# Kernel optimization log

Measured on AMD Instinct MI355X. Metric: run time of the kernel, lower is better.

The kernel has to match this reference:

```python
import jax, jax.numpy as jnp
import numpy as np

N_HEADS = 4
T_OUT = 24  # total T; y has T - t_in steps


def setup_inputs() -> dict:
    key = jax.random.key(0)
    k1, k2, k3, k4 = jax.random.split(key, 4)
    B, t_in, N, C, K = 2, 12, 10000, 16, 17  # K = k + 1 (self)
    x = jax.random.normal(k1, (B, t_in, N, C), dtype=jnp.float32)
    nearest_nodes = jax.random.randint(k2, (N, K), 0, N, dtype=jnp.int32)
    nearest_dists = jax.random.uniform(k3, (N, K), dtype=jnp.float32)
    shrink_w = jax.random.normal(k4, (T_OUT - t_in, t_in * N_HEADS), dtype=jnp.float32) * 0.1
    shrink_b = jnp.zeros((T_OUT - t_in,), dtype=jnp.float32)
    return {"x": x, "nearest_nodes": nearest_nodes, "nearest_dists": nearest_dists,
            "shrink_w": shrink_w, "shrink_b": shrink_b}


def reference(x, nearest_nodes, nearest_dists, shrink_w, shrink_b):
    B, t_in, N, C = x.shape
    H = N_HEADS
    # sigma = nearest_dists.max() / sigma_ratio, with sigma_ratio = 1
    sigma = jnp.max(nearest_dists)
    lam = jnp.arange(1, H + 1, dtype=x.dtype) / H  # (H,)
    # distance weights per head: (N, K, H)
    w = jnp.exp(-(nearest_dists[..., None] ** 2) * lam / (sigma ** 2))
    w = jnp.where((nearest_nodes == -1)[..., None], 0.0, w)
    w = jnp.where(w < 1e-8, 0.0, w)
    # pad node at index N; -1 neighbors map to pad (weight already zero)
    pad_x = jnp.concatenate([x, jnp.zeros_like(x[:, :, :1])], axis=2)  # (B,T,N+1,C)
    idx = jnp.where(nearest_nodes == -1, N, nearest_nodes)  # (N, K)
    g = pad_x[:, :, idx]  # (B, t_in, N, K, C) neighbor gather
    # weighted reduce over neighbor axis -> (B, t_in, N, H, C)
    agg = jnp.einsum('btnkc,nkh->btnhc', g, w)
    # (B, N, C, t_in*H)
    a = jnp.transpose(agg, (0, 2, 4, 1, 3)).reshape(B, N, C, t_in * H)
    y = a @ shrink_w.T + shrink_b  # (B, N, C, T - t_in)
    y = jnp.transpose(y, (0, 3, 1, 2))  # (B, T - t_in, N, C)
    y = jax.nn.selu(y)  # CustomActivationFunction default mode='selu'
    return jnp.concatenate([x, y], axis=1)  # (B, T, N, C)
```

## Files before the change

kernel.cpp:

```cpp
#include <hip/hip_runtime.h>
#include <hip/hip_bf16.h>
#include <math.h>

#define NB      2
#define T_IN    12
#define T_OUT_  24
#define O_OUT   12
#define NN      10000
#define CC      16
#define KK      17
#define HH      4
#define JJ      48
#define PL      24
#define XCHN    40
#define CHN     250
#define XBLK    (PL * XCHN)
#define SBLK    167
#define GN      8
#define GBLK    (NN / GN)
#define PSTRU   34
#define ANSU    (PL * PSTRU)

__device__ __forceinline__ unsigned int f2bf(float f) {
    union { float f; unsigned int u; } v; v.f = f;
    unsigned int r = v.u + 0x7FFFu + ((v.u >> 16) & 1u);
    return r >> 16;
}
__device__ __forceinline__ float bf_lo(unsigned int u) {
    union { unsigned int u; float f; } v; v.u = u << 16; return v.f;
}
__device__ __forceinline__ float bf_hi(unsigned int u) {
    union { unsigned int u; float f; } v; v.u = u & 0xffff0000u; return v.f;
}

__global__ __launch_bounds__(256) void setup_kernel(
    const float* __restrict__ x,
    const float* __restrict__ dists, int ndists,
    float* __restrict__ out,
    unsigned short* __restrict__ xt,
    int* __restrict__ sigma_bits)
{
    const int tid = threadIdx.x;
    if (blockIdx.x < XBLK) {
        const int p  = blockIdx.x / XCHN;
        const int ch = blockIdx.x % XCHN;
        const int b = p / T_IN, t = p % T_IN;
        const int n0 = ch * CHN;
        const float* xp = x + (long)(p * NN + n0) * CC;
        float* op = out + (long)((b * T_OUT_ + t) * NN + n0) * CC;
        uint2* xtp = (uint2*)xt + (long)n0 * (PL * 4) + p * 4;
        for (int i = tid; i < CHN * 4; i += 256) {
            const int nl = i >> 2, q = i & 3;
            const float4 v = *(const float4*)(xp + i * 4);
            *(float4*)(op + i * 4) = v;
            uint2 pk;
            pk.x = f2bf(v.x) | (f2bf(v.y) << 16);
            pk.y = f2bf(v.z) | (f2bf(v.w) << 16);
            xtp[(long)nl * (PL * 4) + q] = pk;
        }
    } else {
        const int sb = blockIdx.x - XBLK;
        float m = 0.0f;
        const int nv4 = ndists >> 2;
        const float4* d4 = (const float4*)dists;
        for (int i = sb * 256 + tid; i < nv4; i += SBLK * 256) {
            float4 v = d4[i];
            m = fmaxf(fmaxf(m, fmaxf(v.x, v.y)), fmaxf(v.z, v.w));
        }
        for (int i = (nv4 << 2) + sb * 256 + tid; i < ndists; i += SBLK * 256)
            m = fmaxf(m, dists[i]);
        #pragma unroll
        for (int off = 32; off > 0; off >>= 1)
            m = fmaxf(m, __shfl_down(m, off, 64));
        __shared__ float sm[4];
        int lane = tid & 63, wid = tid >> 6;
        if (lane == 0) sm[wid] = m;
        __syncthreads();
        if (tid == 0) {
            float mm = fmaxf(fmaxf(sm[0], sm[1]), fmaxf(sm[2], sm[3]));
            atomicMax(sigma_bits, __float_as_int(mm));
        }
    }
}

__global__ __launch_bounds__(384) void fused_kernel(
    const unsigned short* __restrict__ xt,
    const int*   __restrict__ nodes,
    const float* __restrict__ dists,
    const int*   __restrict__ sigma_bits,
    const float* __restrict__ Wm,
    const float* __restrict__ bias,
    float* __restrict__ out)
{
    const int tid = threadIdx.x;
    const int n0  = blockIdx.x * GN;

    __shared__ int      lidx[GN * KK];
    __shared__ float    lw[GN * KK][HH];
    __shared__ float    W_s[O_OUT * JJ];
    __shared__ float    b_s[O_OUT];
    __shared__ unsigned a_s[GN * ANSU];

    for (int i = tid; i < O_OUT * JJ; i += 384) W_s[i] = Wm[i];
    if (tid < O_OUT) b_s[tid] = bias[tid];

    const float sigma  = __int_as_float(*sigma_bits);
    const float inv_s2 = 1.0f / (sigma * sigma);
    if (tid < GN * KK) {
        const int   nd = nodes[n0 * KK + tid];
        const float dd = dists[n0 * KK + tid];
        const float e1 = expf(-dd * dd * inv_s2 * 0.25f);
        float w0 = e1, w1 = e1 * e1, w2 = w1 * e1, w3 = w1 * w1;
        if (nd == -1) { w0 = w1 = w2 = w3 = 0.f; }
        if (w0 < 1e-8f) w0 = 0.f;
        if (w1 < 1e-8f) w1 = 0.f;
        if (w2 < 1e-8f) w2 = 0.f;
        if (w3 < 1e-8f) w3 = 0.f;
        lidx[tid]  = ((nd < 0) ? 0 : nd) * (PL * CC * 2);
        lw[tid][0] = w0; lw[tid][1] = w1; lw[tid][2] = w2; lw[tid][3] = w3;
    }
    __syncthreads();

    const int slot  = tid / 48;
    const int l     = tid % 48;
    const int rb    = slot * KK;
    const int plane = l >> 1;
    const int co    = (l & 1) * 8;
    const char* xtb = (const char*)xt;

    float acc[HH][8];
    #pragma unroll
    for (int h = 0; h < HH; ++h)
        #pragma unroll
        for (int j = 0; j < 8; ++j) acc[h][j] = 0.f;

    #pragma unroll
    for (int k = 0; k < KK; ++k) {
        const uint4  gv = *(const uint4*)(xtb + lidx[rb + k] + (l << 4));
        const float4 wv = *(const float4*)lw[rb + k];
        float g[8];
        g[0] = bf_lo(gv.x); g[1] = bf_hi(gv.x);
        g[2] = bf_lo(gv.y); g[3] = bf_hi(gv.y);
        g[4] = bf_lo(gv.z); g[5] = bf_hi(gv.z);
        g[6] = bf_lo(gv.w); g[7] = bf_hi(gv.w);
        #pragma unroll
        for (int j = 0; j < 8; ++j) {
            acc[0][j] += g[j] * wv.x;
            acc[1][j] += g[j] * wv.y;
            acc[2][j] += g[j] * wv.z;
            acc[3][j] += g[j] * wv.w;
        }
    }

    {
        unsigned* ap = a_s + slot * ANSU + plane * PSTRU + co * 2;
        #pragma unroll
        for (int j = 0; j < 8; ++j) {
            uint2 pk;
            pk.x = f2bf(acc[0][j]) | (f2bf(acc[1][j]) << 16);
            pk.y = f2bf(acc[2][j]) | (f2bf(acc[3][j]) << 16);
            *(uint2*)(ap + j * 2) = pk;
        }
    }
    __syncthreads();

    const float kScale = 1.0507009873554805f;
    const float kAlpha = 1.6732632423543772f;
    #pragma unroll
    for (int jj = 0; jj < 8; ++jj) {
        const int oid = tid + 384 * jj;
        const int c   = oid & 15;
        const int r   = oid >> 4;
        const int o   = r % O_OUT;
        const int rr  = r / O_OUT;
        const int b   = rr & 1;
        const int ns  = rr >> 1;
        const unsigned* abase = a_s + ns * ANSU + (b * T_IN) * PSTRU + c * 2;
        const float*    wb    = W_s + o * JJ;
        float y = b_s[o];
        #pragma unroll
        for (int t = 0; t < T_IN; ++t) {
            const uint2 av = *(const uint2*)(abase + t * PSTRU);
            y += bf_lo(av.x) * wb[t * 4 + 0];
            y += bf_hi(av.x) * wb[t * 4 + 1];
            y += bf_lo(av.y) * wb[t * 4 + 2];
            y += bf_hi(av.y) * wb[t * 4 + 3];
        }
        y = (y > 0.0f) ? kScale * y : kScale * kAlpha * expm1f(y);
        out[((long)(b * T_OUT_ + T_IN + o) * NN + n0 + ns) * CC + c] = y;
    }
}

extern "C" void kernel_launch(void* const* d_in, const int* in_sizes, int n_in,
                              void* d_out, int out_size, void* d_ws, size_t ws_size,
                              hipStream_t stream) {
    const float* x     = (const float*)d_in[0];
    const int*   nodes = (const int*)  d_in[1];
    const float* dists = (const float*)d_in[2];
    const float* Wm    = (const float*)d_in[3];
    const float* bias  = (const float*)d_in[4];
    float* out = (float*)d_out;

    char* ws = (char*)d_ws;
    int*            sigma_bits = (int*)ws;
    unsigned short* xt         = (unsigned short*)(ws + 1024);

    const int ndists = in_sizes[2];
    setup_kernel<<<XBLK + SBLK, 256, 0, stream>>>(x, dists, ndists, out, xt,
                                                  sigma_bits);
    fused_kernel<<<GBLK, 384, 0, stream>>>(xt, nodes, dists, sigma_bits,
                                           Wm, bias, out);
}
```

Measured before the change: 121.9 us.

## Map one node per wavefront with wave-local barrier and fp32 aggregate staging

Reorganizes the fused kernel so each 64-lane wavefront owns one node: 48 lanes do the neighbor gather-reduce, and the whole wave then runs the shrink projection and SELU for that node. Because the data handoff stays within the wave, the second block-wide barrier becomes a wave barrier. Blocks shrink to 256 threads covering 4 nodes, giving 2500 blocks. Other changes: weights and indices are packed into one uint4 record with bf16 weights, aggregates are staged in shared memory as fp32 float4 instead of bf16 pairs, and expm1f is replaced with __expf-1. Costs are 16 idle lanes during the gather, more shared memory per node, and slightly different rounding.

```diff
diff --git a/kernel.cpp b/kernel.cpp
--- a/kernel.cpp
+++ b/kernel.cpp
@@ -16,10 +16,10 @@
 #define CHN     250
 #define XBLK    (PL * XCHN)
 #define SBLK    167
-#define GN      8
-#define GBLK    (NN / GN)
-#define PSTRU   34
-#define ANSU    (PL * PSTRU)
+#define GW      4
+#define GBLK    (NN / GW)
+#define PSTR    68
+#define ANS     (PL * PSTR)
 
 __device__ __forceinline__ unsigned int f2bf(float f) {
     union { float f; unsigned int u; } v; v.f = f;
@@ -31,6 +31,14 @@
 }
 __device__ __forceinline__ float bf_hi(unsigned int u) {
     union { unsigned int u; float f; } v; v.u = u & 0xffff0000u; return v.f;
+}
+
+__device__ __forceinline__ void wave_fence() {
+#if __has_builtin(__builtin_amdgcn_wave_barrier)
+    __builtin_amdgcn_wave_barrier();
+#else
+    __syncthreads();
+#endif
 }
 
 __global__ __launch_bounds__(256) void setup_kernel(
@@ -83,7 +91,7 @@
     }
 }
 
-__global__ __launch_bounds__(384) void fused_kernel(
+__global__ __launch_bounds__(256) void fused_kernel(
     const unsigned short* __restrict__ xt,
     const int*   __restrict__ nodes,
     const float* __restrict__ dists,
@@ -92,21 +100,21 @@
     const float* __restrict__ bias,
     float* __restrict__ out)
 {
-    const int tid = threadIdx.x;
-    const int n0  = blockIdx.x * GN;
-
-    __shared__ int      lidx[GN * KK];
-    __shared__ float    lw[GN * KK][HH];
-    __shared__ float    W_s[O_OUT * JJ];
-    __shared__ float    b_s[O_OUT];
-    __shared__ unsigned a_s[GN * ANSU];
-
-    for (int i = tid; i < O_OUT * JJ; i += 384) W_s[i] = Wm[i];
+    const int tid  = threadIdx.x;
+    const int wave = tid >> 6;
+    const int lane = tid & 63;
+    const int n0   = blockIdx.x * GW;
+
+    __shared__ float W_s[O_OUT * JJ];
+    __shared__ float b_s[O_OUT];
+    __shared__ uint4 lrec[GW * KK];
+    __shared__ float a_s[GW * ANS];
+
+    for (int i = tid; i < O_OUT * JJ; i += 256) W_s[i] = Wm[i];
     if (tid < O_OUT) b_s[tid] = bias[tid];
-
-    const float sigma  = __int_as_float(*sigma_bits);
-    const float inv_s2 = 1.0f / (sigma * sigma);
-    if (tid < GN * KK) {
+    if (tid < GW * KK) {
+        const float sigma  = __int_as_float(*sigma_bits);
+        const float inv_s2 = 1.0f / (sigma * sigma);
         const int   nd = nodes[n0 * KK + tid];
         const float dd = dists[n0 * KK + tid];
         const float e1 = expf(-dd * dd * inv_s2 * 0.25f);
@@ -116,78 +124,76 @@
         if (w1 < 1e-8f) w1 = 0.f;
         if (w2 < 1e-8f) w2 = 0.f;
         if (w3 < 1e-8f) w3 = 0.f;
-        lidx[tid]  = ((nd < 0) ? 0 : nd) * (PL * CC * 2);
-        lw[tid][0] = w0; lw[tid][1] = w1; lw[tid][2] = w2; lw[tid][3] = w3;
+        uint4 rec;
+        rec.x = (unsigned)(((nd < 0) ? 0 : nd) * (PL * CC * 2));
+        rec.y = f2bf(w0) | (f2bf(w1) << 16);
+        rec.z = f2bf(w2) | (f2bf(w3) << 16);
+        rec.w = 0;
+        lrec[tid] = rec;
     }
     __syncthreads();
 
-    const int slot  = tid / 48;
-    const int l     = tid % 48;
-    const int rb    = slot * KK;
-    const int plane = l >> 1;
-    const int co    = (l & 1) * 8;
-    const char* xtb = (const char*)xt;
-
-    float acc[HH][8];
-    #pragma unroll
-    for (int h = 0; h < HH; ++h)
-        #pragma unroll
-        for (int j = 0; j < 8; ++j) acc[h][j] = 0.f;
-
-    #pragma unroll
-    for (int k = 0; k < KK; ++k) {
-        const uint4  gv = *(const uint4*)(xtb + lidx[rb + k] + (l << 4));
-        const float4 wv = *(const float4*)lw[rb + k];
-        float g[8];
-        g[0] = bf_lo(gv.x); g[1] = bf_hi(gv.x);
-        g[2] = bf_lo(gv.y); g[3] = bf_hi(gv.y);
-        g[4] = bf_lo(gv.z); g[5] = bf_hi(gv.z);
-        g[6] = bf_lo(gv.w); g[7] = bf_hi(gv.w);
-        #pragma unroll
-        for (int j = 0; j < 8; ++j) {
-            acc[0][j] += g[j] * wv.x;
-            acc[1][j] += g[j] * wv.y;
-            acc[2][j] += g[j] * wv.z;
-            acc[3][j] += g[j] * wv.w;
-        }
-    }
-
-    {
-        unsigned* ap = a_s + slot * ANSU + plane * PSTRU + co * 2;
-        #pragma unroll
-        for (int j = 0; j < 8; ++j) {
-            uint2 pk;
-            pk.x = f2bf(acc[0][j]) | (f2bf(acc[1][j]) << 16);
-            pk.y = f2bf(acc[2][j]) | (f2bf(acc[3][j]) << 16);
-            *(uint2*)(ap + j * 2) = pk;
-        }
-    }
-    __syncthreads();
+    const int rb = wave * KK;
+    float* abase = a_s + wave * ANS;
+    if (lane < 48) {
+        const char* xtb = (const char*)xt;
+        float acc[HH][8];
+        #pragma unroll
+        for (int h = 0; h < HH; ++h)
+            #pragma unroll
+            for (int j = 0; j < 8; ++j) acc[h][j] = 0.f;
+
+        #pragma unroll
+        for (int k = 0; k < KK; ++k) {
+            const uint4 rec = lrec[rb + k];
+            const uint4 gv  = *(const uint4*)(xtb + rec.x + (lane << 4));
+            const float w0 = bf_lo(rec.y), w1 = bf_hi(rec.y);
+            const float w2 = bf_lo(rec.z), w3 = bf_hi(rec.z);
+            float g[8];
+            g[0] = bf_lo(gv.x); g[1] = bf_hi(gv.x);
+            g[2] = bf_lo(gv.y); g[3] = bf_hi(gv.y);
+            g[4] = bf_lo(gv.z); g[5] = bf_hi(gv.z);
+            g[6] = bf_lo(gv.w); g[7] = bf_hi(gv.w);
+            #pragma unroll
+            for (int j = 0; j < 8; ++j) {
+                acc[0][j] += g[j] * w0;
+                acc[1][j] += g[j] * w1;
+                acc[2][j] += g[j] * w2;
+                acc[3][j] += g[j] * w3;
+            }
+        }
+
+        const int plane = lane >> 1;
+        const int oct   = lane & 1;
+        float* ap = abase + plane * PSTR + oct * 32;
+        #pragma unroll
+        for (int j = 0; j < 8; ++j)
+            *(float4*)(ap + j * 4) =
+                make_float4(acc[0][j], acc[1][j], acc[2][j], acc[3][j]);
+    }
+    wave_fence();
 
     const float kScale = 1.0507009873554805f;
     const float kAlpha = 1.6732632423543772f;
+    const int n = n0 + wave;
+    const int c = lane & 15;
+    const int q = lane >> 4;
     #pragma unroll
-    for (int jj = 0; jj < 8; ++jj) {
-        const int oid = tid + 384 * jj;
-        const int c   = oid & 15;
-        const int r   = oid >> 4;
-        const int o   = r % O_OUT;
-        const int rr  = r / O_OUT;
-        const int b   = rr & 1;
-        const int ns  = rr >> 1;
-        const unsigned* abase = a_s + ns * ANSU + (b * T_IN) * PSTRU + c * 2;
-        const float*    wb    = W_s + o * JJ;
+    for (int r = 0; r < 6; ++r) {
+        const int rr = r * 4 + q;
+        const int o  = rr % O_OUT;
+        const int b  = rr / O_OUT;
+        const float* ab = abase + (b * T_IN) * PSTR + c * 4;
+        const float* wb = W_s + o * JJ;
         float y = b_s[o];
         #pragma unroll
         for (int t = 0; t < T_IN; ++t) {
-            const uint2 av = *(const uint2*)(abase + t * PSTRU);
-            y += bf_lo(av.x) * wb[t * 4 + 0];
-            y += bf_hi(av.x) * wb[t * 4 + 1];
-            y += bf_lo(av.y) * wb[t * 4 + 2];
-            y += bf_hi(av.y) * wb[t * 4 + 3];
-        }
-        y = (y > 0.0f) ? kScale * y : kScale * kAlpha * expm1f(y);
-        out[((long)(b * T_OUT_ + T_IN + o) * NN + n0 + ns) * CC + c] = y;
+            const float4 av = *(const float4*)(ab + t * PSTR);
+            const float4 wv = *(const float4*)(wb + t * 4);
+            y += av.x * wv.x + av.y * wv.y + av.z * wv.z + av.w * wv.w;
+        }
+        y = (y > 0.0f) ? kScale * y : kScale * kAlpha * (__expf(y) - 1.0f);
+        out[((long)(b * T_OUT_ + T_IN + o) * NN + n) * CC + c] = y;
     }
 }
 
@@ -208,6 +214,6 @@
     const int ndists = in_sizes[2];
     setup_kernel<<<XBLK + SBLK, 256, 0, stream>>>(x, dists, ndists, out, xt,
                                                   sigma_bits);
-    fused_kernel<<<GBLK, 384, 0, stream>>>(xt, nodes, dists, sigma_bits,
+    fused_kernel<<<GBLK, 256, 0, stream>>>(xt, nodes, dists, sigma_bits,
                                            Wm, bias, out);
 }
```

After: 111.6 us. 1.09x faster.
